# Performance work log

Hardware: AMD Instinct MI355X
Metric: run time of the kernel (lower is better)

The kernel has to match this reference:

```python
import jax, jax.numpy as jnp
import numpy as np

N, E, D, ED, FD, H, Q, K, G = 50000, 600000, 128, 128, 512, 1, 3, 512, 512
NEG_SLOPE = 0.2
EPS = 1e-5


def setup_inputs() -> dict:
    key = jax.random.key(0)
    ks = jax.random.split(key, 16)
    inp = {
        'x': jax.random.normal(ks[0], (N, D), jnp.float32),
        'edge_index': jax.random.randint(ks[1], (2, E), 0, N, jnp.int32),
        'edge_attr': jax.random.normal(ks[2], (E, ED), jnp.float32),
        'batch_vec': jnp.sort(jax.random.randint(ks[3], (N,), 0, G, jnp.int32)),
        'W_l': jax.random.normal(ks[4], (D, H * D), jnp.float32),
        'b_l': jnp.zeros((H * D,), jnp.float32),
        'W_r': jax.random.normal(ks[5], (D, H * D), jnp.float32),
        'b_r': jnp.zeros((H * D,), jnp.float32),
        'W_edge': jax.random.normal(ks[6], (ED, H * D), jnp.float32),
        'att': jax.random.normal(ks[7], (H, D), jnp.float32),
        'conv_bias': jnp.zeros((H * D,), jnp.float32),
        'adapter_W': jax.random.normal(ks[8], (D, D), jnp.float32),
        'adapter_b': jnp.zeros((D,), jnp.float32),
        'norm_g': jnp.ones((D,), jnp.float32),
        'norm_b': jnp.zeros((D,), jnp.float32),
        'codebooks': jax.random.normal(ks[9], (Q, K, D), jnp.float32),
        'out_W': jax.random.normal(ks[10], (D, FD), jnp.float32),
        'out_b': jnp.zeros((FD,), jnp.float32),
        'outnorm_g': jnp.ones((FD,), jnp.float32),
        'outnorm_b': jnp.zeros((FD,), jnp.float32),
    }
    return inp


def _layer_norm(x, g, b):
    m = x.mean(-1, keepdims=True)
    v = ((x - m) ** 2).mean(-1, keepdims=True)
    return (x - m) * jax.lax.rsqrt(v + EPS) * g + b


def _forward(x, edge_index, edge_attr, batch_vec, W_l, b_l, W_r, b_r, W_edge, att,
             conv_bias, adapter_W, adapter_b, norm_g, norm_b, codebooks, out_W, out_b,
             outnorm_g, outnorm_b):
    sg = jax.lax.stop_gradient
    n = x.shape[0]
    # ---- GATv2Conv (PyG defaults: add_self_loops=True, fill_value='mean') ----
    loops = jnp.arange(n, dtype=edge_index.dtype)
    src = jnp.concatenate([edge_index[0], loops])
    dst = jnp.concatenate([edge_index[1], loops])
    mean_attr = edge_attr.mean(0)
    ea = jnp.concatenate([edge_attr, jnp.broadcast_to(mean_attr, (n, edge_attr.shape[1]))])
    xl = (x @ W_l + b_l).reshape(n, H, D)   # source transform
    xr = (x @ W_r + b_r).reshape(n, H, D)   # target transform
    e_emb = (ea @ W_edge).reshape(-1, H, D)
    e = xl[src] + xr[dst] + e_emb           # [Etot,H,D]
    score = jnp.einsum('ehd,hd->eh', jax.nn.leaky_relu(e, NEG_SLOPE), att)
    smax = jax.ops.segment_max(score, dst, num_segments=n)
    ex = jnp.exp(score - smax[dst])
    denom = jax.ops.segment_sum(ex, dst, num_segments=n)
    alpha = ex / (denom[dst] + 1e-16)       # per-target softmax
    out = jax.ops.segment_sum(xl[src] * alpha[..., None], dst, num_segments=n)  # [n,H,D]
    out = out.reshape(n, H * D) + conv_bias
    h = out.reshape(n, H, D).mean(1)        # mean over heads
    # ---- global mean pool over graphs ----
    sums = jax.ops.segment_sum(h, batch_vec, num_segments=G)
    cnts = jax.ops.segment_sum(jnp.ones((n,), h.dtype), batch_vec, num_segments=G)
    g = sums / jnp.maximum(cnts, 1.0)[:, None]
    # ---- adapter + layernorm ----
    g = g @ adapter_W + adapter_b
    g = _layer_norm(g, norm_g, norm_b)
    # ---- residual VQ (euclidean nearest code, straight-through) ----
    residual = g
    quantized_out = jnp.zeros_like(g)
    codes, idxs, commits = [], [], []
    cb_sq = (codebooks ** 2).sum(-1)        # [Q,K]
    for q in range(Q):
        cb = codebooks[q]
        d2 = (residual ** 2).sum(-1, keepdims=True) - 2.0 * residual @ cb.T + cb_sq[q]
        idx = jnp.argmin(d2, axis=-1)
        code = cb[idx]
        commits.append(((sg(code) - residual) ** 2).mean())
        quantized_out = quantized_out + residual + sg(code - residual)
        codes.append(code)
        idxs.append(idx)
        residual = residual - sg(code)
    commit_loss = jnp.stack(commits).mean()
    residual_loss = ((g - quantized_out) ** 2).mean()
    loss = commit_loss + residual_loss
    indices = jnp.stack(idxs, axis=1)       # [G,Q]
    # ---- per-quantizer straight-through tokens -> projection -> layernorm ----
    tokens = jnp.stack([g + sg(c - g) for c in codes], axis=1)  # [G,Q,D]
    tokens = tokens @ out_W + out_b                              # [G,Q,FD]
    tokens = _layer_norm(tokens, outnorm_g, outnorm_b)
    return tokens, indices, loss


def reference(x, edge_index, edge_attr, batch_vec, W_l, b_l, W_r, b_r, W_edge, att,
              conv_bias, adapter_W, adapter_b, norm_g, norm_b, codebooks, out_W, out_b,
              outnorm_g, outnorm_b):
    return _forward(x, edge_index, edge_attr, batch_vec, W_l, b_l, W_r, b_r, W_edge,
                    att, conv_bias, adapter_W, adapter_b, norm_g, norm_b, codebooks,
                    out_W, out_b, outnorm_g, outnorm_b)
```

## Files before the change

kernel.cpp:

```cpp
#include <hip/hip_runtime.h>
#include <math.h>

#define N_NODES 50000
#define E_EDGES 600000
#define DD 128
#define G_GRAPHS 512
#define K_CODES 512
#define Q_QUANT 3
#define FD_OUT 512
#define NEG_SLOPE 0.2f
#define LN_EPS 1e-5f

static __device__ __forceinline__ float lrelu(float v){ return v > 0.f ? v : NEG_SLOPE*v; }
static __device__ __forceinline__ float wsum(float v){
#pragma unroll
  for (int m = 1; m < 64; m <<= 1) v += __shfl_xor(v, m);
  return v;
}
static __device__ __forceinline__ float wmax(float v){
#pragma unroll
  for (int m = 1; m < 64; m <<= 1) v = fmaxf(v, __shfl_xor(v, m));
  return v;
}

#define EA_LD 130

__global__ __launch_bounds__(256)
void k_xform(const float* __restrict__ x, const float* __restrict__ W,
             const float* __restrict__ bias, float* __restrict__ out, int n)
{
  __shared__ __align__(16) float xt[64*EA_LD];
  __shared__ __align__(16) float Wt[32*128];
  const int tid = threadIdx.x;
  const int r0 = blockIdx.x * 64;
  {
    const int q = tid & 63, eb = tid >> 6;
#pragma unroll
    for (int i = 0; i < 16; ++i){
      int e = eb + 4*i;
      int row = r0 + e;
      float2 v = make_float2(0.f, 0.f);
      if (row < n) v = *(const float2*)&x[row*DD + q*2];
      *(float2*)&xt[e*EA_LD + q*2] = v;
    }
  }
  const int eg = tid >> 4;
  const int cg = tid & 15;
  float acc[4][8];
#pragma unroll
  for (int j = 0; j < 4; ++j)
#pragma unroll
    for (int u = 0; u < 8; ++u) acc[j][u] = 0.f;

  for (int kq = 0; kq < 4; ++kq){
    __syncthreads();
    {
      const int c4 = tid & 31, kb = tid >> 5;
#pragma unroll
      for (int i = 0; i < 4; ++i){
        int kk = kb + 8*i;
        *(float4*)&Wt[kk*128 + c4*4] = *(const float4*)&W[(kq*32+kk)*DD + c4*4];
      }
    }
    __syncthreads();
    const int kb2 = kq*32;
#pragma unroll 4
    for (int k = 0; k < 32; ++k){
      float aa[4];
#pragma unroll
      for (int j = 0; j < 4; ++j) aa[j] = xt[(eg*4+j)*EA_LD + kb2 + k];
      float bb[8];
      *(float4*)&bb[0] = *(const float4*)&Wt[k*128 + cg*4];
      *(float4*)&bb[4] = *(const float4*)&Wt[k*128 + 64 + cg*4];
#pragma unroll
      for (int j = 0; j < 4; ++j)
#pragma unroll
        for (int u = 0; u < 8; ++u) acc[j][u] = fmaf(aa[j], bb[u], acc[j][u]);
    }
  }
  float bv[8];
  *(float4*)&bv[0] = *(const float4*)&bias[cg*4];
  *(float4*)&bv[4] = *(const float4*)&bias[64 + cg*4];
#pragma unroll
  for (int j = 0; j < 4; ++j){
    int row = r0 + eg*4 + j;
    if (row < n){
      float o[8];
#pragma unroll
      for (int u = 0; u < 8; ++u) o[u] = acc[j][u] + bv[u];
      *(float4*)&out[row*DD + cg*4]      = *(const float4*)&o[0];
      *(float4*)&out[row*DD + 64 + cg*4] = *(const float4*)&o[4];
    }
  }
}

__global__ __launch_bounds__(256)
void k_edge(const float* __restrict__ edge_attr, const float* __restrict__ W_edge,
            const int* __restrict__ ei, const float* __restrict__ xl,
            const float* __restrict__ xr, const float* __restrict__ att,
            const int* __restrict__ off, int* __restrict__ pos,
            uint2* __restrict__ rec, float* __restrict__ asum_mid)
{
  __shared__ __align__(16) float ea[64*EA_LD];
  __shared__ __align__(16) float Wt[32*128];
  const int tid = threadIdx.x;
  const int e0 = blockIdx.x * 64;
  {
    const int q = tid & 63, eb = tid >> 6;
#pragma unroll
    for (int i = 0; i < 16; ++i){
      int e = eb + 4*i;
      *(float2*)&ea[e*EA_LD + q*2] = *(const float2*)&edge_attr[(e0+e)*DD + q*2];
    }
  }
  const int eg = tid >> 4;
  const int cg = tid & 15;
  float acc[4][8];
#pragma unroll
  for (int j = 0; j < 4; ++j)
#pragma unroll
    for (int u = 0; u < 8; ++u) acc[j][u] = 0.f;

  for (int kq = 0; kq < 4; ++kq){
    __syncthreads();
    {
      const int c4 = tid & 31, kb = tid >> 5;
#pragma unroll
      for (int i = 0; i < 4; ++i){
        int kk = kb + 8*i;
        *(float4*)&Wt[kk*128 + c4*4] = *(const float4*)&W_edge[(kq*32+kk)*DD + c4*4];
      }
    }
    __syncthreads();
    const int kb2 = kq*32;
#pragma unroll 4
    for (int k = 0; k < 32; ++k){
      float aa[4];
#pragma unroll
      for (int j = 0; j < 4; ++j) aa[j] = ea[(eg*4+j)*EA_LD + kb2 + k];
      float bb[8];
      *(float4*)&bb[0] = *(const float4*)&Wt[k*128 + cg*4];
      *(float4*)&bb[4] = *(const float4*)&Wt[k*128 + 64 + cg*4];
#pragma unroll
      for (int j = 0; j < 4; ++j)
#pragma unroll
        for (int u = 0; u < 8; ++u) acc[j][u] = fmaf(aa[j], bb[u], acc[j][u]);
    }
  }
  float attv[8];
  *(float4*)&attv[0] = *(const float4*)&att[cg*4];
  *(float4*)&attv[4] = *(const float4*)&att[64 + cg*4];
  float sp[4];
  int dsts[4], srcs[4];
#pragma unroll
  for (int j = 0; j < 4; ++j){
    int e = e0 + eg*4 + j;
    int s = ei[e];
    int d = ei[E_EDGES + e];
    srcs[j] = s; dsts[j] = d;
    float xlv[8], xrv[8];
    *(float4*)&xlv[0] = *(const float4*)&xl[s*DD + cg*4];
    *(float4*)&xlv[4] = *(const float4*)&xl[s*DD + 64 + cg*4];
    *(float4*)&xrv[0] = *(const float4*)&xr[d*DD + cg*4];
    *(float4*)&xrv[4] = *(const float4*)&xr[d*DD + 64 + cg*4];
    float p = 0.f;
#pragma unroll
    for (int u = 0; u < 8; ++u){
      float vv = acc[j][u] + xlv[u] + xrv[u];
      p += lrelu(vv) * attv[u];
    }
    sp[j] = p;
  }
#pragma unroll
  for (int m = 1; m < 16; m <<= 1){
#pragma unroll
    for (int j = 0; j < 4; ++j) sp[j] += __shfl_xor(sp[j], m);
  }
  if (cg == 0){
#pragma unroll
    for (int j = 0; j < 4; ++j){
      int d = dsts[j];
      int p = atomicAdd(&pos[d], 1);
      uint2 r;
      r.x = (unsigned)srcs[j];
      r.y = __float_as_uint(sp[j]);
      rec[off[d] + p] = r;
    }
  }
  if (tid < 128){
    float s = 0.f;
    for (int e = 0; e < 64; ++e) s += ea[e*EA_LD + tid];
    atomicAdd(&asum_mid[(blockIdx.x & 63)*DD + tid], s);
  }
}

__global__ __launch_bounds__(128)
void k_me(const float* __restrict__ asum_mid, const float* __restrict__ W_edge,
          float* __restrict__ me)
{
  __shared__ float mean[128];
  const int d = threadIdx.x;
  float s = 0.f;
  for (int r = 0; r < 64; ++r) s += asum_mid[r*DD + d];
  mean[d] = s / (float)E_EDGES;
  __syncthreads();
  float acc = 0.f;
  for (int k = 0; k < 128; ++k) acc += mean[k] * W_edge[k*DD + d];
  me[d] = acc;
}

__global__ __launch_bounds__(256)
void k_hist(const int* __restrict__ ei, int* __restrict__ indeg)
{
  int e = blockIdx.x*256 + threadIdx.x;
  if (e < E_EDGES) atomicAdd(&indeg[ei[E_EDGES + e]], 1);
}

#define SCAN_CH 49
__global__ __launch_bounds__(1024)
void k_scan(const int* __restrict__ indeg, int* __restrict__ off)
{
  __shared__ int sA[1024], sB[1024];
  const int tid = threadIdx.x;
  const int base = tid * SCAN_CH;
  int s = 0;
  for (int i = 0; i < SCAN_CH; ++i){
    int id = base + i;
    if (id < N_NODES) s += indeg[id];
  }
  sA[tid] = s;
  __syncthreads();
  int* src = sA; int* dst = sB;
  for (int d = 1; d < 1024; d <<= 1){
    int v = src[tid] + (tid >= d ? src[tid-d] : 0);
    dst[tid] = v;
    __syncthreads();
    int* t = src; src = dst; dst = t;
  }
  int run = (tid == 0) ? 0 : src[tid-1];
  for (int i = 0; i < SCAN_CH; ++i){
    int id = base + i;
    if (id < N_NODES){ off[id] = run; run += indeg[id]; }
  }
  if (tid == 1023) off[N_NODES] = run;
}

__global__ __launch_bounds__(256)
void k_aggregate(const int* __restrict__ off, const uint2* __restrict__ rec,
                 const float* __restrict__ xl, const float* __restrict__ xr,
                 const float* __restrict__ me, const float* __restrict__ att,
                 const float* __restrict__ conv_bias, const int* __restrict__ batch_vec,
                 float* __restrict__ gsum, float* __restrict__ gcnt)
{
  __shared__ float hshare[4][128];
  __shared__ int bsh[4];
  const int tid = threadIdx.x, lane = tid & 63, wid = tid >> 6;
  const int i = blockIdx.x*4 + wid;
  float2 xli = *(const float2*)&xl[i*DD + lane*2];
  float2 xri = *(const float2*)&xr[i*DD + lane*2];
  float2 mev = *(const float2*)&me[lane*2];
  float2 attv = *(const float2*)&att[lane*2];
  float v0 = xli.x + xri.x + mev.x;
  float v1 = xli.y + xri.y + mev.y;
  float s_self = wsum(lrelu(v0)*attv.x + lrelu(v1)*attv.y);
  const int o0 = off[i], o1 = off[i+1];
  const int deg = o1 - o0;
  uint2 myrec = make_uint2(0u, __float_as_uint(-INFINITY));
  float m = s_self;
  if (lane < deg) myrec = rec[o0 + lane];
  m = fmaxf(m, __uint_as_float(myrec.y));
  for (int b = 64; b < deg; b += 64){
    int j = b + lane;
    if (j < deg) m = fmaxf(m, __uint_as_float(rec[o0 + j].y));
  }
  m = wmax(m);
  float wse = __expf(s_self - m);
  float den = wse;
  float a0 = wse * xli.x, a1 = wse * xli.y;
  if (deg <= 64){
    float msc = __uint_as_float(myrec.y);
    int msrc = (int)myrec.x;
#pragma unroll 2
    for (int j = 0; j < deg; ++j){
      float sc = __shfl(msc, j);
      int s = __shfl(msrc, j);
      float w = __expf(sc - m);
      den += w;
      float2 xs = *(const float2*)&xl[s*DD + lane*2];
      a0 = fmaf(w, xs.x, a0);
      a1 = fmaf(w, xs.y, a1);
    }
  } else {
#pragma unroll 2
    for (int j = 0; j < deg; ++j){
      uint2 r = rec[o0 + j];
      float w = __expf(__uint_as_float(r.y) - m);
      den += w;
      float2 xs = *(const float2*)&xl[(int)r.x*DD + lane*2];
      a0 = fmaf(w, xs.x, a0);
      a1 = fmaf(w, xs.y, a1);
    }
  }
  float inv = 1.0f / (den + 1e-16f);
  float2 cb2 = *(const float2*)&conv_bias[lane*2];
  float h0 = a0*inv + cb2.x;
  float h1 = a1*inv + cb2.y;
  int b = batch_vec[i];
  hshare[wid][lane*2]     = h0;
  hshare[wid][lane*2 + 1] = h1;
  if (lane == 0) bsh[wid] = b;
  __syncthreads();
  bool uni = (bsh[0]==bsh[1]) && (bsh[1]==bsh[2]) && (bsh[2]==bsh[3]);
  if (uni){
    if (wid == 0){
      float s0 = hshare[0][lane*2] + hshare[1][lane*2] + hshare[2][lane*2] + hshare[3][lane*2];
      float s1 = hshare[0][lane*2+1] + hshare[1][lane*2+1] + hshare[2][lane*2+1] + hshare[3][lane*2+1];
      atomicAdd(&gsum[b*DD + lane*2],     s0);
      atomicAdd(&gsum[b*DD + lane*2 + 1], s1);
      if (lane == 0) atomicAdd(&gcnt[b], 4.0f);
    }
  } else {
    atomicAdd(&gsum[b*DD + lane*2],     h0);
    atomicAdd(&gsum[b*DD + lane*2 + 1], h1);
    if (lane == 0) atomicAdd(&gcnt[b], 1.0f);
  }
}

__global__ __launch_bounds__(128)
void k_pool(const float* __restrict__ gsum, const float* __restrict__ gcnt,
            const float* __restrict__ aW, const float* __restrict__ ab,
            const float* __restrict__ ng, const float* __restrict__ nb,
            float* __restrict__ g_ln)
{
  __shared__ float row[128];
  __shared__ float red[128];
  const int g = blockIdx.x, d = threadIdx.x;
  float denom = fmaxf(gcnt[g], 1.0f);
  row[d] = gsum[g*DD + d] / denom;
  __syncthreads();
  double accd = (double)ab[d];
  for (int k = 0; k < 128; ++k) accd += (double)row[k] * (double)aW[k*DD + d];
  float a = (float)accd;
  red[d] = a; __syncthreads();
  for (int s = 64; s > 0; s >>= 1){ if (d < s) red[d] += red[d+s]; __syncthreads(); }
  float mean = red[0] / 128.f; __syncthreads();
  float c = a - mean;
  red[d] = c*c; __syncthreads();
  for (int s = 64; s > 0; s >>= 1){ if (d < s) red[d] += red[d+s]; __syncthreads(); }
  float var = red[0] / 128.f; __syncthreads();
  float inv = (float)(1.0 / sqrt((double)var + (double)LN_EPS));
  g_ln[g*DD + d] = c * inv * ng[d] + nb[d];
}

__global__ __launch_bounds__(256)
void k_rvq(const float* __restrict__ g_ln, const float* __restrict__ codebooks,
           float* __restrict__ ind_out, int* __restrict__ idx_i,
           float* __restrict__ accs)
{
  __shared__ __align__(16) float r_lds[128];
  __shared__ float red[128];
  __shared__ double bd[64];
  __shared__ int bi[64];
  __shared__ int chosen;
  const int g = blockIdx.x, tid = threadIdx.x;
  if (tid < 128) r_lds[tid] = g_ln[g*DD + tid];
  __syncthreads();
  const int cl = tid >> 2, dq = tid & 3;
  for (int q = 0; q < Q_QUANT; ++q){
    const float* cb = codebooks + (size_t)q * K_CODES * DD;
    double bestd = 1e300; int besti = 1 << 30;
    for (int r = 0; r < 8; ++r){
      int c = r*64 + cl;
      double rc = 0.0, cc = 0.0;
      const float4* cp = (const float4*)&cb[c*DD + dq*32];
      const float4* rp = (const float4*)&r_lds[dq*32];
#pragma unroll
      for (int i = 0; i < 8; ++i){
        float4 cv = cp[i]; float4 rv = rp[i];
        rc += (double)cv.x*rv.x + (double)cv.y*rv.y + (double)cv.z*rv.z + (double)cv.w*rv.w;
        cc += (double)cv.x*cv.x + (double)cv.y*cv.y + (double)cv.z*cv.z + (double)cv.w*cv.w;
      }
      rc += __shfl_xor(rc, 1); rc += __shfl_xor(rc, 2);
      cc += __shfl_xor(cc, 1); cc += __shfl_xor(cc, 2);
      if (dq == 0){
        double d2 = cc - 2.0*rc;
        if (d2 < bestd || (d2 == bestd && c < besti)){ bestd = d2; besti = c; }
      }
    }
    if (dq == 0){ bd[cl] = bestd; bi[cl] = besti; }
    __syncthreads();
    if (tid < 64){
      double d2 = bd[tid]; int ii = bi[tid];
#pragma unroll
      for (int m = 1; m < 64; m <<= 1){
        double od = __shfl_xor(d2, m); int oi = __shfl_xor(ii, m);
        if (od < d2 || (od == d2 && oi < ii)){ d2 = od; ii = oi; }
      }
      if (tid == 0) chosen = ii;
    }
    __syncthreads();
    const int idx = chosen;
    if (tid == 0){
      ind_out[g*Q_QUANT + q] = (float)idx;
      idx_i[g*Q_QUANT + q] = idx;
    }
    if (tid < 128){
      float cd = cb[idx*DD + tid];
      float diff = cd - r_lds[tid];
      red[tid] = diff * diff;
      r_lds[tid] -= cd;
    }
    __syncthreads();
    for (int s = 64; s > 0; s >>= 1){ if (tid < s) red[tid] += red[tid+s]; __syncthreads(); }
    if (tid == 0) atomicAdd(&accs[q], red[0]);
    __syncthreads();
  }
  if (tid < 128) red[tid] = r_lds[tid]*r_lds[tid];
  __syncthreads();
  for (int s = 64; s > 0; s >>= 1){ if (tid < s) red[tid] += red[tid+s]; __syncthreads(); }
  if (tid == 0) atomicAdd(&accs[3], red[0]);
}

__global__ __launch_bounds__(256)
void k_tokens(const float* __restrict__ codebooks, const int* __restrict__ idx_i,
              const float* __restrict__ out_W, const float* __restrict__ out_b,
              const float* __restrict__ og, const float* __restrict__ ob,
              float* __restrict__ tokens)
{
  __shared__ __align__(16) float c_lds[128];
  __shared__ float red[256];
  const int blk = blockIdx.x;
  const int g = blk / 3, q = blk % 3;
  const int tid = threadIdx.x;
  const int idx = idx_i[g*Q_QUANT + q];
  if (tid < 128) c_lds[tid] = codebooks[((size_t)q*K_CODES + idx)*DD + tid];
  __syncthreads();
  double v0 = (double)out_b[tid];
  double v1 = (double)out_b[tid + 256];
  for (int k = 0; k < 128; ++k){
    double ck = (double)c_lds[k];
    v0 += ck * (double)out_W[k*FD_OUT + tid];
    v1 += ck * (double)out_W[k*FD_OUT + tid + 256];
  }
  float f0 = (float)v0, f1 = (float)v1;
  red[tid] = f0 + f1; __syncthreads();
  for (int s = 128; s > 0; s >>= 1){ if (tid < s) red[tid] += red[tid+s]; __syncthreads(); }
  float mean = red[0] / 512.f; __syncthreads();
  float d0 = f0 - mean, d1 = f1 - mean;
  red[tid] = d0*d0 + d1*d1; __syncthreads();
  for (int s = 128; s > 0; s >>= 1){ if (tid < s) red[tid] += red[tid+s]; __syncthreads(); }
  float var = red[0] / 512.f; __syncthreads();
  float inv = (float)(1.0 / sqrt((double)var + (double)LN_EPS));
  tokens[(size_t)blk*FD_OUT + tid]       = d0*inv*og[tid] + ob[tid];
  tokens[(size_t)blk*FD_OUT + tid + 256] = d1*inv*og[tid+256] + ob[tid+256];
}

__global__ void k_loss(const float* __restrict__ accs, float* __restrict__ out)
{
  float commit = (accs[0] + accs[1] + accs[2]) / (3.0f * G_GRAPHS * DD);
  float resid  = accs[3] / ((float)G_GRAPHS * DD);
  out[0] = commit + resid;
}

extern "C" void kernel_launch(void* const* d_in, const int* in_sizes, int n_in,
                              void* d_out, int out_size, void* d_ws, size_t ws_size,
                              hipStream_t stream)
{
  (void)in_sizes; (void)n_in; (void)out_size; (void)ws_size;
  const float* x         = (const float*)d_in[0];
  const int*   ei        = (const int*)d_in[1];
  const float* edge_attr = (const float*)d_in[2];
  const int*   batch_vec = (const int*)d_in[3];
  const float* W_l       = (const float*)d_in[4];
  const float* b_l       = (const float*)d_in[5];
  const float* W_r       = (const float*)d_in[6];
  const float* b_r       = (const float*)d_in[7];
  const float* W_edge    = (const float*)d_in[8];
  const float* att       = (const float*)d_in[9];
  const float* conv_bias = (const float*)d_in[10];
  const float* aW        = (const float*)d_in[11];
  const float* ab        = (const float*)d_in[12];
  const float* ng        = (const float*)d_in[13];
  const float* nb        = (const float*)d_in[14];
  const float* codebooks = (const float*)d_in[15];
  const float* out_W     = (const float*)d_in[16];
  const float* out_b     = (const float*)d_in[17];
  const float* og        = (const float*)d_in[18];
  const float* ob        = (const float*)d_in[19];
  float* outf = (float*)d_out;

  char* w = (char*)d_ws;
  size_t o = 0;
  auto nxt = [&](size_t bytes)->void*{
    void* p = w + o;
    o += (bytes + 511) & ~(size_t)511;
    return p;
  };
  int*   indeg    = (int*)  nxt((size_t)N_NODES*4);
  int*   pos      = (int*)  nxt((size_t)N_NODES*4);
  float* asum_mid = (float*)nxt((size_t)64*DD*4);
  float* gsum     = (float*)nxt((size_t)G_GRAPHS*DD*4);
  float* gcnt     = (float*)nxt((size_t)G_GRAPHS*4);
  float* accs     = (float*)nxt(16);
  const size_t zero_span = o;
  int*   off      = (int*)  nxt((size_t)(N_NODES+1)*4);
  float* xl       = (float*)nxt((size_t)N_NODES*DD*4);
  float* xr       = (float*)nxt((size_t)N_NODES*DD*4);
  uint2* rec      = (uint2*)nxt((size_t)E_EDGES*8);
  float* me       = (float*)nxt((size_t)DD*4);
  float* g_ln     = (float*)nxt((size_t)G_GRAPHS*DD*4);
  int*   idx_i    = (int*)  nxt((size_t)G_GRAPHS*Q_QUANT*4);

  hipMemsetAsync(w, 0, zero_span, stream);

  k_hist<<<dim3((E_EDGES+255)/256), dim3(256), 0, stream>>>(ei, indeg);
  k_scan<<<dim3(1), dim3(1024), 0, stream>>>(indeg, off);
  k_xform<<<dim3((N_NODES+63)/64), dim3(256), 0, stream>>>(x, W_l, b_l, xl, N_NODES);
  k_xform<<<dim3((N_NODES+63)/64), dim3(256), 0, stream>>>(x, W_r, b_r, xr, N_NODES);
  k_edge<<<dim3(E_EDGES/64), dim3(256), 0, stream>>>(edge_attr, W_edge, ei, xl, xr, att,
                                                     off, pos, rec, asum_mid);
  k_me<<<dim3(1), dim3(128), 0, stream>>>(asum_mid, W_edge, me);
  k_aggregate<<<dim3(N_NODES/4), dim3(256), 0, stream>>>(off, rec, xl, xr, me, att,
                                                         conv_bias, batch_vec, gsum, gcnt);
  k_pool<<<dim3(G_GRAPHS), dim3(128), 0, stream>>>(gsum, gcnt, aW, ab, ng, nb, g_ln);
  k_rvq<<<dim3(G_GRAPHS), dim3(256), 0, stream>>>(g_ln, codebooks,
                                                  outf + (size_t)G_GRAPHS*Q_QUANT*FD_OUT,
                                                  idx_i, accs);
  k_tokens<<<dim3(G_GRAPHS*Q_QUANT), dim3(256), 0, stream>>>(codebooks, idx_i, out_W, out_b,
                                                             og, ob, outf);
  k_loss<<<dim3(1), dim3(1), 0, stream>>>(accs,
                                          outf + (size_t)G_GRAPHS*Q_QUANT*FD_OUT
                                               + (size_t)G_GRAPHS*Q_QUANT);
}
```

Measured before the change: 672.9 us.

## Fuse xl/xr transforms, prefetch weight tiles, parallelize scan, tune unroll and bounds

Merges the two node-transform launches into one kernel that reads x once and produces both xl and xr. Both it and the edge GEMM now prefetch the next weight slice into registers while computing on the current one, and take two k-steps per inner iteration. The single-block 1024-thread scan becomes a three-kernel multi-block scan. Aggregation loop unroll and launch bounds occupancy hints are also raised. The fused kernel holds twice the accumulators, so register pressure and spills are a risk.

New measurement: 665.3 us. About the same (-1.1%).

```diff
diff --git a/kernel.cpp b/kernel.cpp
--- a/kernel.cpp
+++ b/kernel.cpp
@@ -25,14 +25,18 @@
 
 #define EA_LD 130
 
-__global__ __launch_bounds__(256)
-void k_xform(const float* __restrict__ x, const float* __restrict__ W,
-             const float* __restrict__ bias, float* __restrict__ out, int n)
+__global__ __launch_bounds__(256, 2)
+void k_xform2(const float* __restrict__ x,
+              const float* __restrict__ W_l, const float* __restrict__ b_l,
+              const float* __restrict__ W_r, const float* __restrict__ b_r,
+              float* __restrict__ xl, float* __restrict__ xr, int n)
 {
   __shared__ __align__(16) float xt[64*EA_LD];
-  __shared__ __align__(16) float Wt[32*128];
+  __shared__ __align__(16) float WtL[32*128];
+  __shared__ __align__(16) float WtR[32*128];
   const int tid = threadIdx.x;
   const int r0 = blockIdx.x * 64;
+  const int c4 = tid & 31, kb = tid >> 5;
   {
     const int q = tid & 63, eb = tid >> 6;
 #pragma unroll
@@ -43,58 +47,95 @@
       if (row < n) v = *(const float2*)&x[row*DD + q*2];
       *(float2*)&xt[e*EA_LD + q*2] = v;
     }
-  }
+    float4 w0L[4], w0R[4];
+#pragma unroll
+    for (int i = 0; i < 4; ++i){
+      w0L[i] = *(const float4*)&W_l[(kb + 8*i)*DD + c4*4];
+      w0R[i] = *(const float4*)&W_r[(kb + 8*i)*DD + c4*4];
+    }
+#pragma unroll
+    for (int i = 0; i < 4; ++i){
+      *(float4*)&WtL[(kb + 8*i)*128 + c4*4] = w0L[i];
+      *(float4*)&WtR[(kb + 8*i)*128 + c4*4] = w0R[i];
+    }
+  }
+  __syncthreads();
+
   const int eg = tid >> 4;
   const int cg = tid & 15;
-  float acc[4][8];
+  float accL[4][8], accR[4][8];
 #pragma unroll
   for (int j = 0; j < 4; ++j)
 #pragma unroll
-    for (int u = 0; u < 8; ++u) acc[j][u] = 0.f;
+    for (int u = 0; u < 8; ++u){ accL[j][u] = 0.f; accR[j][u] = 0.f; }
 
   for (int kq = 0; kq < 4; ++kq){
-    __syncthreads();
-    {
-      const int c4 = tid & 31, kb = tid >> 5;
+    float4 wregL[4], wregR[4];
+    if (kq < 3){
 #pragma unroll
       for (int i = 0; i < 4; ++i){
-        int kk = kb + 8*i;
-        *(float4*)&Wt[kk*128 + c4*4] = *(const float4*)&W[(kq*32+kk)*DD + c4*4];
+        wregL[i] = *(const float4*)&W_l[((kq+1)*32 + kb + 8*i)*DD + c4*4];
+        wregR[i] = *(const float4*)&W_r[((kq+1)*32 + kb + 8*i)*DD + c4*4];
       }
     }
-    __syncthreads();
     const int kb2 = kq*32;
-#pragma unroll 4
-    for (int k = 0; k < 32; ++k){
-      float aa[4];
-#pragma unroll
-      for (int j = 0; j < 4; ++j) aa[j] = xt[(eg*4+j)*EA_LD + kb2 + k];
-      float bb[8];
-      *(float4*)&bb[0] = *(const float4*)&Wt[k*128 + cg*4];
-      *(float4*)&bb[4] = *(const float4*)&Wt[k*128 + 64 + cg*4];
+    for (int kp = 0; kp < 16; ++kp){
+      float2 aa[4];
 #pragma unroll
       for (int j = 0; j < 4; ++j)
-#pragma unroll
-        for (int u = 0; u < 8; ++u) acc[j][u] = fmaf(aa[j], bb[u], acc[j][u]);
-    }
-  }
-  float bv[8];
-  *(float4*)&bv[0] = *(const float4*)&bias[cg*4];
-  *(float4*)&bv[4] = *(const float4*)&bias[64 + cg*4];
+        aa[j] = *(const float2*)&xt[(eg*4+j)*EA_LD + kb2 + kp*2];
+      float bL[16], bR[16];
+      *(float4*)&bL[0]  = *(const float4*)&WtL[(kp*2)*128 + cg*4];
+      *(float4*)&bL[4]  = *(const float4*)&WtL[(kp*2)*128 + 64 + cg*4];
+      *(float4*)&bL[8]  = *(const float4*)&WtL[(kp*2+1)*128 + cg*4];
+      *(float4*)&bL[12] = *(const float4*)&WtL[(kp*2+1)*128 + 64 + cg*4];
+      *(float4*)&bR[0]  = *(const float4*)&WtR[(kp*2)*128 + cg*4];
+      *(float4*)&bR[4]  = *(const float4*)&WtR[(kp*2)*128 + 64 + cg*4];
+      *(float4*)&bR[8]  = *(const float4*)&WtR[(kp*2+1)*128 + cg*4];
+      *(float4*)&bR[12] = *(const float4*)&WtR[(kp*2+1)*128 + 64 + cg*4];
+#pragma unroll
+      for (int j = 0; j < 4; ++j){
+#pragma unroll
+        for (int u = 0; u < 8; ++u) accL[j][u] = fmaf(aa[j].x, bL[u],   accL[j][u]);
+#pragma unroll
+        for (int u = 0; u < 8; ++u) accL[j][u] = fmaf(aa[j].y, bL[8+u], accL[j][u]);
+#pragma unroll
+        for (int u = 0; u < 8; ++u) accR[j][u] = fmaf(aa[j].x, bR[u],   accR[j][u]);
+#pragma unroll
+        for (int u = 0; u < 8; ++u) accR[j][u] = fmaf(aa[j].y, bR[8+u], accR[j][u]);
+      }
+    }
+    if (kq < 3){
+      __syncthreads();
+#pragma unroll
+      for (int i = 0; i < 4; ++i){
+        *(float4*)&WtL[(kb + 8*i)*128 + c4*4] = wregL[i];
+        *(float4*)&WtR[(kb + 8*i)*128 + c4*4] = wregR[i];
+      }
+      __syncthreads();
+    }
+  }
+  float bvL[8], bvR[8];
+  *(float4*)&bvL[0] = *(const float4*)&b_l[cg*4];
+  *(float4*)&bvL[4] = *(const float4*)&b_l[64 + cg*4];
+  *(float4*)&bvR[0] = *(const float4*)&b_r[cg*4];
+  *(float4*)&bvR[4] = *(const float4*)&b_r[64 + cg*4];
 #pragma unroll
   for (int j = 0; j < 4; ++j){
     int row = r0 + eg*4 + j;
     if (row < n){
-      float o[8];
-#pragma unroll
-      for (int u = 0; u < 8; ++u) o[u] = acc[j][u] + bv[u];
-      *(float4*)&out[row*DD + cg*4]      = *(const float4*)&o[0];
-      *(float4*)&out[row*DD + 64 + cg*4] = *(const float4*)&o[4];
-    }
-  }
-}
-
-__global__ __launch_bounds__(256)
+      float oL[8], oR[8];
+#pragma unroll
+      for (int u = 0; u < 8; ++u){ oL[u] = accL[j][u] + bvL[u]; oR[u] = accR[j][u] + bvR[u]; }
+      *(float4*)&xl[row*DD + cg*4]      = *(const float4*)&oL[0];
+      *(float4*)&xl[row*DD + 64 + cg*4] = *(const float4*)&oL[4];
+      *(float4*)&xr[row*DD + cg*4]      = *(const float4*)&oR[0];
+      *(float4*)&xr[row*DD + 64 + cg*4] = *(const float4*)&oR[4];
+    }
+  }
+}
+
+__global__ __launch_bounds__(256, 3)
 void k_edge(const float* __restrict__ edge_attr, const float* __restrict__ W_edge,
             const int* __restrict__ ei, const float* __restrict__ xl,
             const float* __restrict__ xr, const float* __restrict__ att,
@@ -105,6 +146,7 @@
   __shared__ __align__(16) float Wt[32*128];
   const int tid = threadIdx.x;
   const int e0 = blockIdx.x * 64;
+  const int c4 = tid & 31, kb = tid >> 5;
   {
     const int q = tid & 63, eb = tid >> 6;
 #pragma unroll
@@ -112,7 +154,16 @@
       int e = eb + 4*i;
       *(float2*)&ea[e*EA_LD + q*2] = *(const float2*)&edge_attr[(e0+e)*DD + q*2];
     }
-  }
+    float4 w0[4];
+#pragma unroll
+    for (int i = 0; i < 4; ++i)
+      w0[i] = *(const float4*)&W_edge[(kb + 8*i)*DD + c4*4];
+#pragma unroll
+    for (int i = 0; i < 4; ++i)
+      *(float4*)&Wt[(kb + 8*i)*128 + c4*4] = w0[i];
+  }
+  __syncthreads();
+
   const int eg = tid >> 4;
   const int cg = tid & 15;
   float acc[4][8];
@@ -122,29 +173,38 @@
     for (int u = 0; u < 8; ++u) acc[j][u] = 0.f;
 
   for (int kq = 0; kq < 4; ++kq){
-    __syncthreads();
-    {
-      const int c4 = tid & 31, kb = tid >> 5;
-#pragma unroll
-      for (int i = 0; i < 4; ++i){
-        int kk = kb + 8*i;
-        *(float4*)&Wt[kk*128 + c4*4] = *(const float4*)&W_edge[(kq*32+kk)*DD + c4*4];
+    float4 wreg[4];
+    if (kq < 3){
+#pragma unroll
+      for (int i = 0; i < 4; ++i)
+        wreg[i] = *(const float4*)&W_edge[((kq+1)*32 + kb + 8*i)*DD + c4*4];
+    }
+    const int kb2 = kq*32;
+#pragma unroll 2
+    for (int kp = 0; kp < 16; ++kp){
+      float2 aa[4];
+#pragma unroll
+      for (int j = 0; j < 4; ++j)
+        aa[j] = *(const float2*)&ea[(eg*4+j)*EA_LD + kb2 + kp*2];
+      float bb[16];
+      *(float4*)&bb[0]  = *(const float4*)&Wt[(kp*2)*128 + cg*4];
+      *(float4*)&bb[4]  = *(const float4*)&Wt[(kp*2)*128 + 64 + cg*4];
+      *(float4*)&bb[8]  = *(const float4*)&Wt[(kp*2+1)*128 + cg*4];
+      *(float4*)&bb[12] = *(const float4*)&Wt[(kp*2+1)*128 + 64 + cg*4];
+#pragma unroll
+      for (int j = 0; j < 4; ++j){
+#pragma unroll
+        for (int u = 0; u < 8; ++u) acc[j][u] = fmaf(aa[j].x, bb[u],   acc[j][u]);
+#pragma unroll
+        for (int u = 0; u < 8; ++u) acc[j][u] = fmaf(aa[j].y, bb[8+u], acc[j][u]);
       }
     }
-    __syncthreads();
-    const int kb2 = kq*32;
-#pragma unroll 4
-    for (int k = 0; k < 32; ++k){
-      float aa[4];
-#pragma unroll
-      for (int j = 0; j < 4; ++j) aa[j] = ea[(eg*4+j)*EA_LD + kb2 + k];
-      float bb[8];
-      *(float4*)&bb[0] = *(const float4*)&Wt[k*128 + cg*4];
-      *(float4*)&bb[4] = *(const float4*)&Wt[k*128 + 64 + cg*4];
-#pragma unroll
-      for (int j = 0; j < 4; ++j)
-#pragma unroll
-        for (int u = 0; u < 8; ++u) acc[j][u] = fmaf(aa[j], bb[u], acc[j][u]);
+    if (kq < 3){
+      __syncthreads();
+#pragma unroll
+      for (int i = 0; i < 4; ++i)
+        *(float4*)&Wt[(kb + 8*i)*128 + c4*4] = wreg[i];
+      __syncthreads();
     }
   }
   float attv[8];
@@ -216,33 +276,49 @@
   if (e < E_EDGES) atomicAdd(&indeg[ei[E_EDGES + e]], 1);
 }
 
-#define SCAN_CH 49
-__global__ __launch_bounds__(1024)
-void k_scan(const int* __restrict__ indeg, int* __restrict__ off)
-{
-  __shared__ int sA[1024], sB[1024];
+#define SC_NB ((N_NODES + 511) / 512)
+__global__ __launch_bounds__(512)
+void k_scan1(const int* __restrict__ indeg, int* __restrict__ off, int* __restrict__ bsum)
+{
+  __shared__ int s[512];
   const int tid = threadIdx.x;
-  const int base = tid * SCAN_CH;
-  int s = 0;
-  for (int i = 0; i < SCAN_CH; ++i){
-    int id = base + i;
-    if (id < N_NODES) s += indeg[id];
-  }
-  sA[tid] = s;
-  __syncthreads();
-  int* src = sA; int* dst = sB;
-  for (int d = 1; d < 1024; d <<= 1){
-    int v = src[tid] + (tid >= d ? src[tid-d] : 0);
-    dst[tid] = v;
-    __syncthreads();
-    int* t = src; src = dst; dst = t;
-  }
-  int run = (tid == 0) ? 0 : src[tid-1];
-  for (int i = 0; i < SCAN_CH; ++i){
-    int id = base + i;
-    if (id < N_NODES){ off[id] = run; run += indeg[id]; }
-  }
-  if (tid == 1023) off[N_NODES] = run;
+  const int gid = blockIdx.x*512 + tid;
+  int v = (gid < N_NODES) ? indeg[gid] : 0;
+  s[tid] = v;
+  __syncthreads();
+  for (int d = 1; d < 512; d <<= 1){
+    int t = (tid >= d) ? s[tid-d] : 0;
+    __syncthreads();
+    s[tid] += t;
+    __syncthreads();
+  }
+  if (gid < N_NODES) off[gid] = s[tid] - v;
+  if (tid == 511) bsum[blockIdx.x] = s[511];
+}
+
+__global__ __launch_bounds__(128)
+void k_scan2(const int* __restrict__ bsum, int* __restrict__ boff)
+{
+  __shared__ int s[128];
+  const int tid = threadIdx.x;
+  int v = (tid < SC_NB) ? bsum[tid] : 0;
+  s[tid] = v;
+  __syncthreads();
+  for (int d = 1; d < 128; d <<= 1){
+    int t = (tid >= d) ? s[tid-d] : 0;
+    __syncthreads();
+    s[tid] += t;
+    __syncthreads();
+  }
+  if (tid < SC_NB) boff[tid] = s[tid] - v;
+}
+
+__global__ __launch_bounds__(512)
+void k_scan3(int* __restrict__ off, const int* __restrict__ boff)
+{
+  const int gid = blockIdx.x*512 + threadIdx.x;
+  if (gid < N_NODES) off[gid] += boff[blockIdx.x];
+  if (gid == 0) off[N_NODES] = E_EDGES;
 }
 
 __global__ __launch_bounds__(256)
@@ -280,7 +356,7 @@
   if (deg <= 64){
     float msc = __uint_as_float(myrec.y);
     int msrc = (int)myrec.x;
-#pragma unroll 2
+#pragma unroll 4
     for (int j = 0; j < deg; ++j){
       float sc = __shfl(msc, j);
       int s = __shfl(msrc, j);
@@ -291,7 +367,7 @@
       a1 = fmaf(w, xs.y, a1);
     }
   } else {
-#pragma unroll 2
+#pragma unroll 4
     for (int j = 0; j < deg; ++j){
       uint2 r = rec[o0 + j];
       float w = __expf(__uint_as_float(r.y) - m);
@@ -510,13 +586,17 @@
   float* me       = (float*)nxt((size_t)DD*4);
   float* g_ln     = (float*)nxt((size_t)G_GRAPHS*DD*4);
   int*   idx_i    = (int*)  nxt((size_t)G_GRAPHS*Q_QUANT*4);
+  int*   bsum     = (int*)  nxt((size_t)SC_NB*4);
+  int*   boff     = (int*)  nxt((size_t)SC_NB*4);
 
   hipMemsetAsync(w, 0, zero_span, stream);
 
   k_hist<<<dim3((E_EDGES+255)/256), dim3(256), 0, stream>>>(ei, indeg);
-  k_scan<<<dim3(1), dim3(1024), 0, stream>>>(indeg, off);
-  k_xform<<<dim3((N_NODES+63)/64), dim3(256), 0, stream>>>(x, W_l, b_l, xl, N_NODES);
-  k_xform<<<dim3((N_NODES+63)/64), dim3(256), 0, stream>>>(x, W_r, b_r, xr, N_NODES);
+  k_scan1<<<dim3(SC_NB), dim3(512), 0, stream>>>(indeg, off, bsum);
+  k_scan2<<<dim3(1), dim3(128), 0, stream>>>(bsum, boff);
+  k_scan3<<<dim3(SC_NB), dim3(512), 0, stream>>>(off, boff);
+  k_xform2<<<dim3((N_NODES+63)/64), dim3(256), 0, stream>>>(x, W_l, b_l, W_r, b_r,
+                                                            xl, xr, N_NODES);
   k_edge<<<dim3(E_EDGES/64), dim3(256), 0, stream>>>(edge_attr, W_edge, ei, xl, xr, att,
                                                      off, pos, rec, asum_mid);
   k_me<<<dim3(1), dim3(128), 0, stream>>>(asum_mid, W_edge, me);
```
